# Kernel tuning notes

Hardware: AMD Instinct MI355X
Metric: run time of the kernel (lower is better)

Reference implementation:

```python
import jax, jax.numpy as jnp
import numpy as np

ATT, WEMB, VIEW, ADIM, EMB = 312, 512, 16, 2048, 2048
B = 2048
IN = ATT + WEMB + VIEW * WEMB  # 9016; output_dim defaults to input_dim
EPS = 1e-8  # torch cosine_similarity eps


def setup_inputs() -> dict:
    key = jax.random.key(0)
    ks = jax.random.split(key, 8)
    s = 0.02
    return {
        "x": jax.random.normal(ks[0], (B, IN), dtype=jnp.float32),
        "Wq": s * jax.random.normal(ks[1], (WEMB, ADIM), dtype=jnp.float32),
        "bq": jnp.zeros((ADIM,), jnp.float32),
        "Wk": s * jax.random.normal(ks[2], (WEMB, ADIM), dtype=jnp.float32),
        "bk": jnp.zeros((ADIM,), jnp.float32),
        "Wv": s * jax.random.normal(ks[3], (WEMB, ADIM), dtype=jnp.float32),
        "bv": jnp.zeros((ADIM,), jnp.float32),
        "Wm": s * jax.random.normal(ks[4], (ATT + ADIM, EMB), dtype=jnp.float32),
        "bm": jnp.zeros((EMB,), jnp.float32),
        "Wd1": s * jax.random.normal(ks[5], (EMB, 4096), dtype=jnp.float32),
        "bd1": jnp.zeros((4096,), jnp.float32),
        "Wd2": s * jax.random.normal(ks[6], (4096, IN), dtype=jnp.float32),
        "bd2": jnp.zeros((IN,), jnp.float32),
    }


def reference(x, Wq, bq, Wk, bk, Wv, bv, Wm, bm, Wd1, bd1, Wd2, bd2):
    att_emb = x[:, :ATT]                                   # [B, 312]
    desc_emb = x[:, ATT:ATT + WEMB]                        # [B, 512]
    gpt_emb = x[:, ATT + WEMB:].reshape(x.shape[0], -1, WEMB)  # [B, V, 512]

    # q is the same projected desc for every view (expand before linear)
    q = desc_emb @ Wq + bq                                 # [B, A]
    k = jnp.einsum("bvw,wa->bva", gpt_emb, Wk) + bk        # [B, V, A]
    v = jnp.einsum("bvw,wa->bva", gpt_emb, Wv) + bv        # [B, V, A]

    # cosed score: cosine similarity * L2 distance
    dot = jnp.einsum("bva,ba->bv", k, q)                   # [B, V]
    qn = jnp.maximum(jnp.linalg.norm(q, axis=-1), EPS)     # [B]
    kn = jnp.maximum(jnp.linalg.norm(k, axis=-1), EPS)     # [B, V]
    cs = dot / (qn[:, None] * kn)
    ed = jnp.linalg.norm(q[:, None, :] - k, axis=-1)       # [B, V]
    attn = jax.nn.softmax(cs * ed, axis=-1)                # [B, V]

    # torch.matmul([B,V], [B,V,A]) -> [B,B,A]; .mean(dim=1) averages over the
    # attn-batch axis, i.e. fused[j] = mean_b(attn[b]) @ v[j]. Compute the
    # mathematically identical form without the BxBxA intermediate.
    attn_mean = attn.mean(axis=0)                          # [V]
    fused = jnp.einsum("v,bva->ba", attn_mean, v)          # [B, A]

    z = jax.nn.relu(jnp.concatenate([att_emb, fused], axis=1) @ Wm + bm)  # [B, EMB]
    h = jax.nn.relu(z @ Wd1 + bd1)                          # [B, 4096]
    return h @ Wd2 + bd2                                    # [B, IN]
```

## Files before the change

kernel.cpp:

```cpp
#include <hip/hip_runtime.h>


typedef __bf16 bf16x8 __attribute__((ext_vector_type(8)));
typedef float  f32x4  __attribute__((ext_vector_type(4)));
typedef unsigned short u16;

#define ATT   312
#define WEMB  512
#define VIEW  16
#define ADIM  2048
#define EMB   2048
#define BATCH 2048
#define INDIM 9016
#define KCAT  2360
#define KCATP 2432
#define NOUT  9016
#define NOUTP 9216

__device__ __forceinline__ u16 f2bf(float f) {
  unsigned u = __builtin_bit_cast(unsigned, f);
  u += 0x7FFFu + ((u >> 16) & 1u);
  return (u16)(u >> 16);
}

__device__ __forceinline__ void gl_lds16(const u16* g, u16* l) {
  __builtin_amdgcn_global_load_lds((const __attribute__((address_space(1))) void*)g,
                                   (__attribute__((address_space(3))) void*)l, 16, 0, 0);
}

__global__ void castx_k(const float* __restrict__ x, u16* __restrict__ cc,
                        u16* __restrict__ desc, u16* __restrict__ gpt) {
  const int b = blockIdx.x, t = threadIdx.x;
  const float4* row = (const float4*)(x + (size_t)b * INDIM);
  for (int c = t; c < INDIM / 4; c += 256) {
    float4 v = row[c];
    ushort4 o = make_ushort4(f2bf(v.x), f2bf(v.y), f2bf(v.z), f2bf(v.w));
    if (c < ATT / 4)                 *(ushort4*)&cc[(size_t)b * KCATP + c * 4] = o;
    else if (c < (ATT + WEMB) / 4)   *(ushort4*)&desc[(size_t)b * WEMB + (c - ATT / 4) * 4] = o;
    else                             *(ushort4*)&gpt[(size_t)b * (VIEW * WEMB) + (c - (ATT + WEMB) / 4) * 4] = o;
  }
}

__global__ void transcast_k(const float* __restrict__ src, u16* __restrict__ dst,
                            int K, int N, int Kp, int Np) {
  __shared__ float tile[64][65];
  const int k0 = blockIdx.y * 64, n0 = blockIdx.x * 64;
  const int t = threadIdx.x;
  const int tr = t >> 4, tc4 = (t & 15) * 4;
#pragma unroll
  for (int i = 0; i < 4; ++i) {
    const int k = k0 + tr + i * 16;
    float v0 = 0.f, v1 = 0.f, v2 = 0.f, v3 = 0.f;
    if (k < K) {
      const int n = n0 + tc4;
      const float* p = src + (size_t)k * N + n;
      if (n + 3 < N) { float4 v = *(const float4*)p; v0 = v.x; v1 = v.y; v2 = v.z; v3 = v.w; }
      else {
        if (n + 0 < N) v0 = p[0];
        if (n + 1 < N) v1 = p[1];
        if (n + 2 < N) v2 = p[2];
        if (n + 3 < N) v3 = p[3];
      }
    }
    tile[tr + i * 16][tc4 + 0] = v0;
    tile[tr + i * 16][tc4 + 1] = v1;
    tile[tr + i * 16][tc4 + 2] = v2;
    tile[tr + i * 16][tc4 + 3] = v3;
  }
  __syncthreads();
#pragma unroll
  for (int i = 0; i < 4; ++i) {
    const int rn = tr + i * 16;
    const int n = n0 + rn;
    const int kk = k0 + tc4;
    if (n < Np) {
      const bool nv = (n < N);
      ushort4 o = make_ushort4(f2bf(nv ? tile[tc4 + 0][rn] : 0.f),
                               f2bf(nv ? tile[tc4 + 1][rn] : 0.f),
                               f2bf(nv ? tile[tc4 + 2][rn] : 0.f),
                               f2bf(nv ? tile[tc4 + 3][rn] : 0.f));
      *(ushort4*)&dst[(size_t)n * Kp + kk] = o;
    }
  }
}

__device__ __forceinline__ void stage_half(const u16* __restrict__ src, int ld,
                                           u16* dst, int wave, int lane) {
#pragma unroll
  for (int j = 0; j < 2; ++j) {
    const int s = wave * 2 + j;
    const int r = ((s >> 1) << 4) + (lane >> 2);
    const int c = ((s & 1) << 5) +
                  (((lane & 3) << 3) ^ (((lane >> 5) & 1) << 4));
    gl_lds16(src + (long)r * ld + c, dst + s * 512 + (lane << 3));
  }
}

#define BAR   __builtin_amdgcn_s_barrier()
#define LGKM0 asm volatile("s_waitcnt lgkmcnt(0)" ::: "memory")
#define VM6   asm volatile("s_waitcnt vmcnt(6)" ::: "memory")
#define VM0   asm volatile("s_waitcnt vmcnt(0)" ::: "memory")

#define RDA(bufo) do { _Pragma("unroll") for (int mf = 0; mf < 8; ++mf) \
  _Pragma("unroll") for (int kk = 0; kk < 2; ++kk) \
    a[mf][kk] = *(const bf16x8*)&lds[(bufo) + aoff0 + (mf * 2 + kk) * 512]; } while (0)
#define RDB(bufo, nfa, nfb) do { _Pragma("unroll") for (int nf = (nfa); nf <= (nfb); ++nf) \
  _Pragma("unroll") for (int kk = 0; kk < 2; ++kk) \
    b[nf][kk] = *(const bf16x8*)&lds[(bufo) + boff0 + nf * 1024 + kk * 512]; } while (0)
#define QUAD(qm, qn) do { __builtin_amdgcn_s_setprio(1); \
  _Pragma("unroll") for (int m4 = 0; m4 < 4; ++m4) \
  _Pragma("unroll") for (int n2 = 0; n2 < 2; ++n2) \
  _Pragma("unroll") for (int kk = 0; kk < 2; ++kk) \
    acc[(qm) * 4 + m4][(qn) * 2 + n2] = __builtin_amdgcn_mfma_f32_16x16x32_bf16( \
        a[(qm) * 4 + m4][kk], b[(qn) * 2 + n2][kk], acc[(qm) * 4 + m4][(qn) * 2 + n2], 0, 0, 0); \
  __builtin_amdgcn_s_setprio(0); } while (0)

template <int MODE, bool RELU>
__global__ __launch_bounds__(512, 2)
void gemm256(const u16* __restrict__ A, const u16* __restrict__ BT,
             const float* __restrict__ bias, int K, int Nreal,
             float* __restrict__ dstF, u16* __restrict__ dstH, int ldc,
             const float* __restrict__ qbuf, float* __restrict__ dotb,
             float* __restrict__ kn2b, int mt, int nt, int fastm) {
  __shared__ alignas(16) u16 lds[65536];
  const int nwg = mt * nt;
  const int xcd = blockIdx.x & 7, idx = blockIdx.x >> 3;
  const int qq = nwg >> 3, rr = nwg & 7;
  const int wg = (xcd < rr ? xcd * (qq + 1) : rr * (qq + 1) + (xcd - rr) * qq) + idx;
  int tm, tn;
  if (fastm) { tm = wg % mt; tn = wg / mt; } else { tn = wg % nt; tm = wg / nt; }

  const int tid = threadIdx.x;
  const int wave = tid >> 6, lane = tid & 63;
  const long m0 = (long)tm * 256, n0 = (long)tn * 256;
  const int wm = wave >> 2, wn = wave & 3;
  const u16* Ab = A + m0 * K;
  const u16* Bb = BT + n0 * K;

  f32x4 acc[8][4] = {};
  bf16x8 a[8][2], b[4][2];
  const int LP = (lane & 15) * 32 + ((((lane >> 4) << 3)) ^ (((lane >> 3) & 1) << 4));
  const int aoff0 = wm * 8192 + LP;
  const int boff0 = 16384 + (wn >> 1) * 8192 + (wn & 1) * 4096 + LP;
  const int NT = K >> 6;

  stage_half(Ab,               K, &lds[0],     wave, lane);
  stage_half(Ab + 128 * K,     K, &lds[8192],  wave, lane);
  stage_half(Bb,               K, &lds[16384], wave, lane);
  stage_half(Bb + 128 * K,     K, &lds[24576], wave, lane);
  stage_half(Ab + 64,          K, &lds[32768], wave, lane);
  stage_half(Ab + 128 * K + 64, K, &lds[40960], wave, lane);
  stage_half(Bb + 64,          K, &lds[49152], wave, lane);
  VM6; BAR;

  const int iters = NT >> 1;
  for (int i = 0; i < iters; ++i) {
    const int t0 = 2 * i;
    const bool nl = (i < iters - 1);
    RDA(0); RDB(0, 0, 1);
    stage_half(Bb + 128 * K + (t0 + 1) * 64, K, &lds[57344], wave, lane);
    BAR; LGKM0; QUAD(0, 0); BAR;
    RDB(0, 2, 3);
    if (nl) stage_half(Ab + (t0 + 2) * 64, K, &lds[0], wave, lane);
    BAR; LGKM0; QUAD(1, 0); BAR;
    if (nl) stage_half(Ab + 128 * K + (t0 + 2) * 64, K, &lds[8192], wave, lane);
    BAR; QUAD(0, 1); BAR;
    if (nl) stage_half(Bb + (t0 + 2) * 64, K, &lds[16384], wave, lane);
    BAR; QUAD(1, 1);
    if (nl) { VM6; } else { VM0; }
    BAR;
    RDA(32768); RDB(32768, 0, 1);
    if (nl) stage_half(Bb + 128 * K + (t0 + 2) * 64, K, &lds[24576], wave, lane);
    BAR; LGKM0; QUAD(0, 0); BAR;
    RDB(32768, 2, 3);
    if (nl) stage_half(Ab + (t0 + 3) * 64, K, &lds[32768], wave, lane);
    BAR; LGKM0; QUAD(1, 0); BAR;
    if (nl) stage_half(Ab + 128 * K + (t0 + 3) * 64, K, &lds[40960], wave, lane);
    BAR; QUAD(0, 1); BAR;
    if (nl) stage_half(Bb + (t0 + 3) * 64, K, &lds[49152], wave, lane);
    BAR; QUAD(1, 1);
    if (nl) VM6;
    BAR;
  }

  const int lr = lane >> 4, lc = lane & 15;
  if (MODE == 2) {
#pragma unroll
    for (int mf = 0; mf < 8; ++mf) {
#pragma unroll
      for (int r = 0; r < 4; ++r) {
        const long grow = m0 + wm * 128 + mf * 16 + lr * 4 + r;
        const long bb = grow >> 4;
        float ds = 0.f, ks = 0.f;
#pragma unroll
        for (int nf = 0; nf < 4; ++nf) {
          const long col = n0 + wn * 64 + nf * 16 + lc;
          float kv = acc[mf][nf][r] + bias[col];
          ds += kv * qbuf[bb * ADIM + col];
          ks += kv * kv;
        }
#pragma unroll
        for (int m = 1; m < 16; m <<= 1) {
          ds += __shfl_xor(ds, m, 64);
          ks += __shfl_xor(ks, m, 64);
        }
        if (lc == 0) {
          atomicAdd(&dotb[grow], ds);
          atomicAdd(&kn2b[grow], ks);
        }
      }
    }
  } else {
#pragma unroll
    for (int mf = 0; mf < 8; ++mf) {
#pragma unroll
      for (int nf = 0; nf < 4; ++nf) {
        const long col = n0 + wn * 64 + nf * 16 + lc;
        if (col < Nreal) {
          const float bv_ = bias[col];
#pragma unroll
          for (int r = 0; r < 4; ++r) {
            const long row = m0 + wm * 128 + mf * 16 + lr * 4 + r;
            float v = acc[mf][nf][r] + bv_;
            if (RELU) v = fmaxf(v, 0.f);
            if (MODE == 0) dstF[row * (long)ldc + col] = v;
            else           dstH[row * (long)ldc + col] = f2bf(v);
          }
        }
      }
    }
  }
}

template <int MODE, bool RELU>
__global__ __launch_bounds__(256, 2)
void gemm_bt(const u16* __restrict__ A, const u16* __restrict__ BT,
             const float* __restrict__ bias, int K, int Nreal,
             float* __restrict__ dstF, u16* __restrict__ dstH, int ldc,
             int mt, int nt, int fastm) {
  __shared__ alignas(16) u16 Ash[128 * 64];
  __shared__ alignas(16) u16 Bsh[128 * 64];
  const int nwg = mt * nt;
  const int xcd = blockIdx.x & 7, idx = blockIdx.x >> 3;
  const int qq = nwg >> 3, rr = nwg & 7;
  const int wg = (xcd < rr ? xcd * (qq + 1) : rr * (qq + 1) + (xcd - rr) * qq) + idx;
  int tm, tn;
  if (fastm) { tm = wg % mt; tn = wg / mt; } else { tn = wg % nt; tm = wg / nt; }

  const int tid = threadIdx.x;
  const int wave = tid >> 6, lane = tid & 63;
  const long m0 = (long)tm * 128;
  const long n0 = (long)tn * 128;
  const int wm = wave >> 1, wnn = wave & 1;
  f32x4 acc[4][4] = {};

  const int srow = (wave << 5) + (lane >> 3);
  const int scol = (lane & 7) << 3;

  for (int k0 = 0; k0 < K; k0 += 64) {
    __syncthreads();
#pragma unroll
    for (int i = 0; i < 4; ++i) {
      const int r = srow + i * 8;
      gl_lds16(A + (m0 + r) * (long)K + k0 + scol, &Ash[r * 64 + scol]);
      gl_lds16(BT + (n0 + r) * (long)K + k0 + scol, &Bsh[r * 64 + scol]);
    }
    __syncthreads();
#pragma unroll
    for (int kb = 0; kb < 2; ++kb) {
      bf16x8 af[4], bfv[4];
#pragma unroll
      for (int f = 0; f < 4; ++f) {
        af[f]  = *(const bf16x8*)&Ash[(wm * 64 + f * 16 + (lane & 15)) * 64 + kb * 32 + (lane >> 4) * 8];
        bfv[f] = *(const bf16x8*)&Bsh[(wnn * 64 + f * 16 + (lane & 15)) * 64 + kb * 32 + (lane >> 4) * 8];
      }
#pragma unroll
      for (int mf = 0; mf < 4; ++mf)
#pragma unroll
        for (int nf = 0; nf < 4; ++nf)
          acc[mf][nf] = __builtin_amdgcn_mfma_f32_16x16x32_bf16(af[mf], bfv[nf], acc[mf][nf], 0, 0, 0);
    }
  }

  const int lr = lane >> 4, lc = lane & 15;
#pragma unroll
  for (int mf = 0; mf < 4; ++mf) {
#pragma unroll
    for (int nf = 0; nf < 4; ++nf) {
      const long col = n0 + wnn * 64 + nf * 16 + lc;
      if (col < Nreal) {
        const float bv_ = bias[col];
#pragma unroll
        for (int r = 0; r < 4; ++r) {
          const long row = m0 + wm * 64 + mf * 16 + lr * 4 + r;
          float v = acc[mf][nf][r] + bv_;
          if (RELU) v = fmaxf(v, 0.f);
          if (MODE == 0) dstF[row * (long)ldc + col] = v;
          else           dstH[row * (long)ldc + col] = f2bf(v);
        }
      }
    }
  }
}

__global__ void qnorm_k(const float* __restrict__ q, float* __restrict__ qn2) {
  const int b = blockIdx.x, t = threadIdx.x;
  const float4* row = (const float4*)(q + (size_t)b * ADIM);
  float s = 0.f;
#pragma unroll
  for (int i = 0; i < 2; ++i) {
    float4 v = row[t + i * 256];
    s += v.x * v.x + v.y * v.y + v.z * v.z + v.w * v.w;
  }
#pragma unroll
  for (int m = 1; m < 64; m <<= 1) s += __shfl_xor(s, m, 64);
  __shared__ float wsum[4];
  if ((t & 63) == 0) wsum[t >> 6] = s;
  __syncthreads();
  if (t == 0) qn2[b] = wsum[0] + wsum[1] + wsum[2] + wsum[3];
}

__global__ void attn_k(const float* __restrict__ dotb, const float* __restrict__ kn2b,
                       const float* __restrict__ qn2, float* __restrict__ asum) {
  const int b = blockIdx.x * 256 + threadIdx.x;
  const int lane = threadIdx.x & 63;
  const float q2 = qn2[b];
  const float qn = fmaxf(sqrtf(q2), 1e-8f);
  float lg[VIEW];
  float mx = -1e30f;
#pragma unroll
  for (int v = 0; v < VIEW; ++v) {
    const float d = dotb[b * VIEW + v], k2 = kn2b[b * VIEW + v];
    const float kn = fmaxf(sqrtf(k2), 1e-8f);
    const float cs = d / (qn * kn);
    const float ed = sqrtf(fmaxf(q2 - 2.f * d + k2, 0.f));
    lg[v] = cs * ed;
    mx = fmaxf(mx, lg[v]);
  }
  float s = 0.f;
#pragma unroll
  for (int v = 0; v < VIEW; ++v) { lg[v] = expf(lg[v] - mx); s += lg[v]; }
  const float inv = 1.f / s;
#pragma unroll
  for (int v = 0; v < VIEW; ++v) {
    float aa = lg[v] * inv;
#pragma unroll
    for (int m = 1; m < 64; m <<= 1) aa += __shfl_xor(aa, m, 64);
    if (lane == 0) atomicAdd(&asum[v], aa);
  }
}

__global__ void gtilde_k(const u16* __restrict__ gpt, const float* __restrict__ asum,
                         u16* __restrict__ g) {
  const int b = blockIdx.x, t = threadIdx.x;
  float am[VIEW];
#pragma unroll
  for (int v = 0; v < VIEW; ++v) am[v] = asum[v] * (1.f / (float)BATCH);
  float s[8] = {};
  const u16* gx = gpt + (size_t)b * (VIEW * WEMB) + t * 8;
#pragma unroll
  for (int v = 0; v < VIEW; ++v) {
    bf16x8 gv = *(const bf16x8*)&gx[v * WEMB];
#pragma unroll
    for (int j = 0; j < 8; ++j) s[j] += am[v] * (float)gv[j];
  }
  ushort4 o0, o1;
  o0 = make_ushort4(f2bf(s[0]), f2bf(s[1]), f2bf(s[2]), f2bf(s[3]));
  o1 = make_ushort4(f2bf(s[4]), f2bf(s[5]), f2bf(s[6]), f2bf(s[7]));
  *(ushort4*)&g[(size_t)b * WEMB + t * 8] = o0;
  *(ushort4*)&g[(size_t)b * WEMB + t * 8 + 4] = o1;
}

extern "C" void kernel_launch(void* const* d_in, const int* in_sizes, int n_in,
                              void* d_out, int out_size, void* d_ws, size_t ws_size,
                              hipStream_t stream) {
  const float* x   = (const float*)d_in[0];
  const float* Wq  = (const float*)d_in[1];
  const float* bq  = (const float*)d_in[2];
  const float* Wk  = (const float*)d_in[3];
  const float* bk  = (const float*)d_in[4];
  const float* Wv  = (const float*)d_in[5];
  const float* bv  = (const float*)d_in[6];
  const float* Wm  = (const float*)d_in[7];
  const float* bm  = (const float*)d_in[8];
  const float* Wd1 = (const float*)d_in[9];
  const float* bd1 = (const float*)d_in[10];
  const float* Wd2 = (const float*)d_in[11];
  const float* bd2 = (const float*)d_in[12];
  float* out = (float*)d_out;

  char* ws = (char*)d_ws;
  size_t off = 0;
  auto alloc = [&](size_t bytes) -> void* {
    void* p = ws + off;
    off = (off + bytes + 255) & ~(size_t)255;
    return p;
  };
  u16* WqT  = (u16*)alloc((size_t)ADIM * WEMB * 2);
  u16* WkT  = (u16*)alloc((size_t)ADIM * WEMB * 2);
  u16* WvT  = (u16*)alloc((size_t)ADIM * WEMB * 2);
  u16* WmT  = (u16*)alloc((size_t)EMB * KCATP * 2);
  u16* Wd1T = (u16*)alloc((size_t)4096 * EMB * 2);
  u16* Wd2T = (u16*)alloc((size_t)NOUTP * 4096 * 2);
  u16* desc = (u16*)alloc((size_t)BATCH * WEMB * 2);
  u16* gpt  = (u16*)alloc((size_t)BATCH * VIEW * WEMB * 2);
  u16* cc   = (u16*)alloc((size_t)BATCH * KCATP * 2);
  float* q    = (float*)alloc((size_t)BATCH * ADIM * 4);
  float* qn2  = (float*)alloc((size_t)BATCH * 4);
  float* stats = (float*)alloc((size_t)(BATCH * VIEW * 2 + 64) * 4);
  float* dotb = stats;
  float* kn2b = stats + BATCH * VIEW;
  float* asum = stats + BATCH * VIEW * 2;
  u16* gt = (u16*)alloc((size_t)BATCH * WEMB * 2);
  u16* z  = (u16*)alloc((size_t)BATCH * EMB * 2);
  u16* h  = (u16*)alloc((size_t)BATCH * 4096 * 2);
  if (off > ws_size) return;

  hipMemsetAsync(stats, 0, (size_t)(BATCH * VIEW * 2 + 64) * 4, stream);
  hipMemsetAsync(cc, 0, (size_t)BATCH * KCATP * 2, stream);

  castx_k<<<BATCH, 256, 0, stream>>>(x, cc, desc, gpt);

  transcast_k<<<dim3(ADIM / 64, WEMB / 64), 256, 0, stream>>>(Wq, WqT, WEMB, ADIM, WEMB, ADIM);
  transcast_k<<<dim3(ADIM / 64, WEMB / 64), 256, 0, stream>>>(Wk, WkT, WEMB, ADIM, WEMB, ADIM);
  transcast_k<<<dim3(ADIM / 64, WEMB / 64), 256, 0, stream>>>(Wv, WvT, WEMB, ADIM, WEMB, ADIM);
  transcast_k<<<dim3(EMB / 64, KCATP / 64), 256, 0, stream>>>(Wm, WmT, KCAT, EMB, KCATP, EMB);
  transcast_k<<<dim3(4096 / 64, EMB / 64), 256, 0, stream>>>(Wd1, Wd1T, EMB, 4096, EMB, 4096);
  transcast_k<<<dim3(NOUTP / 64, 4096 / 64), 256, 0, stream>>>(Wd2, Wd2T, 4096, NOUT, 4096, NOUTP);

  gemm_bt<0, false><<<16 * 16, 256, 0, stream>>>(
      desc, WqT, bq, WEMB, ADIM, q, nullptr, ADIM, BATCH / 128, ADIM / 128, 0);
  qnorm_k<<<BATCH, 256, 0, stream>>>(q, qn2);
  gemm256<2, false><<<128 * 8, 512, 0, stream>>>(
      gpt, WkT, bk, WEMB, ADIM, nullptr, nullptr, 0, q, dotb, kn2b,
      BATCH * VIEW / 256, ADIM / 256, 0);
  attn_k<<<BATCH / 256, 256, 0, stream>>>(dotb, kn2b, qn2, asum);
  gtilde_k<<<BATCH, 64, 0, stream>>>(gpt, asum, gt);
  gemm_bt<1, false><<<16 * 16, 256, 0, stream>>>(
      gt, WvT, bv, WEMB, ADIM, nullptr, cc + ATT, KCATP, BATCH / 128, ADIM / 128, 0);
  gemm_bt<1, true><<<16 * 16, 256, 0, stream>>>(
      cc, WmT, bm, KCATP, EMB, nullptr, z, EMB, BATCH / 128, EMB / 128, 0);
  gemm256<1, true><<<8 * 16, 512, 0, stream>>>(
      z, Wd1T, bd1, EMB, 4096, nullptr, h, 4096, nullptr, nullptr, nullptr,
      BATCH / 256, 4096 / 256, 0);
  gemm256<0, false><<<8 * 36, 512, 0, stream>>>(
      h, Wd2T, bd2, 4096, NOUT, out, nullptr, NOUT, nullptr, nullptr, nullptr,
      BATCH / 256, NOUTP / 256, 1);
}
```

Measured before the change: 700.3 us.

## Split-K the two decoder GEMMs with fp32 atomic accumulation

Adds a K-split parameter to the 256x256 GEMM kernel so the Wd1 and Wd2 GEMMs launch 2x and 4x more workgroups. Each slice atomically adds its partial sums into a zeroed fp32 buffer, and only the first slice adds the bias. Because ReLU can no longer run in the epilogue, a separate kernel applies ReLU and casts the fp32 hidden activations to bf16. The aim is to fix poor CU occupancy and tail effects from the small tile counts, at the cost of extra memsets, atomic traffic, a larger fp32 intermediate that reuses the dead desc/gpt workspace, and nondeterministic summation order.

```diff
diff --git a/kernel.cpp b/kernel.cpp
--- a/kernel.cpp
+++ b/kernel.cpp
@@ -115,42 +115,45 @@
         a[(qm) * 4 + m4][kk], b[(qn) * 2 + n2][kk], acc[(qm) * 4 + m4][(qn) * 2 + n2], 0, 0, 0); \
   __builtin_amdgcn_s_setprio(0); } while (0)
 
-template <int MODE, bool RELU>
+template <int MODE>
 __global__ __launch_bounds__(512, 2)
 void gemm256(const u16* __restrict__ A, const u16* __restrict__ BT,
              const float* __restrict__ bias, int K, int Nreal,
-             float* __restrict__ dstF, u16* __restrict__ dstH, int ldc,
+             float* __restrict__ dstF, int ldc,
              const float* __restrict__ qbuf, float* __restrict__ dotb,
-             float* __restrict__ kn2b, int mt, int nt, int fastm) {
+             float* __restrict__ kn2b, int mt, int nt, int fastm,
+             int ks, int kl) {
   __shared__ alignas(16) u16 lds[65536];
-  const int nwg = mt * nt;
+  const int nwg = mt * nt * ks;
   const int xcd = blockIdx.x & 7, idx = blockIdx.x >> 3;
   const int qq = nwg >> 3, rr = nwg & 7;
   const int wg = (xcd < rr ? xcd * (qq + 1) : rr * (qq + 1) + (xcd - rr) * qq) + idx;
+  const int ksl = wg % ks;
+  const int rem = wg / ks;
   int tm, tn;
-  if (fastm) { tm = wg % mt; tn = wg / mt; } else { tn = wg % nt; tm = wg / nt; }
+  if (fastm) { tm = rem % mt; tn = rem / mt; } else { tn = rem % nt; tm = rem / nt; }
 
   const int tid = threadIdx.x;
   const int wave = tid >> 6, lane = tid & 63;
   const long m0 = (long)tm * 256, n0 = (long)tn * 256;
   const int wm = wave >> 2, wn = wave & 3;
-  const u16* Ab = A + m0 * K;
-  const u16* Bb = BT + n0 * K;
+  const u16* Ab = A + m0 * K + (long)ksl * kl;
+  const u16* Bb = BT + n0 * K + (long)ksl * kl;
 
   f32x4 acc[8][4] = {};
   bf16x8 a[8][2], b[4][2];
   const int LP = (lane & 15) * 32 + ((((lane >> 4) << 3)) ^ (((lane >> 3) & 1) << 4));
   const int aoff0 = wm * 8192 + LP;
   const int boff0 = 16384 + (wn >> 1) * 8192 + (wn & 1) * 4096 + LP;
-  const int NT = K >> 6;
-
-  stage_half(Ab,               K, &lds[0],     wave, lane);
-  stage_half(Ab + 128 * K,     K, &lds[8192],  wave, lane);
-  stage_half(Bb,               K, &lds[16384], wave, lane);
-  stage_half(Bb + 128 * K,     K, &lds[24576], wave, lane);
-  stage_half(Ab + 64,          K, &lds[32768], wave, lane);
+  const int NT = kl >> 6;
+
+  stage_half(Ab,                K, &lds[0],     wave, lane);
+  stage_half(Ab + 128 * K,      K, &lds[8192],  wave, lane);
+  stage_half(Bb,                K, &lds[16384], wave, lane);
+  stage_half(Bb + 128 * K,      K, &lds[24576], wave, lane);
+  stage_half(Ab + 64,           K, &lds[32768], wave, lane);
   stage_half(Ab + 128 * K + 64, K, &lds[40960], wave, lane);
-  stage_half(Bb + 64,          K, &lds[49152], wave, lane);
+  stage_half(Bb + 64,           K, &lds[49152], wave, lane);
   VM6; BAR;
 
   const int iters = NT >> 1;
@@ -191,22 +194,22 @@
       for (int r = 0; r < 4; ++r) {
         const long grow = m0 + wm * 128 + mf * 16 + lr * 4 + r;
         const long bb = grow >> 4;
-        float ds = 0.f, ks = 0.f;
+        float ds = 0.f, ks2 = 0.f;
 #pragma unroll
         for (int nf = 0; nf < 4; ++nf) {
           const long col = n0 + wn * 64 + nf * 16 + lc;
           float kv = acc[mf][nf][r] + bias[col];
           ds += kv * qbuf[bb * ADIM + col];
-          ks += kv * kv;
+          ks2 += kv * kv;
         }
 #pragma unroll
         for (int m = 1; m < 16; m <<= 1) {
           ds += __shfl_xor(ds, m, 64);
-          ks += __shfl_xor(ks, m, 64);
+          ks2 += __shfl_xor(ks2, m, 64);
         }
         if (lc == 0) {
           atomicAdd(&dotb[grow], ds);
-          atomicAdd(&kn2b[grow], ks);
+          atomicAdd(&kn2b[grow], ks2);
         }
       }
     }
@@ -217,19 +220,28 @@
       for (int nf = 0; nf < 4; ++nf) {
         const long col = n0 + wn * 64 + nf * 16 + lc;
         if (col < Nreal) {
-          const float bv_ = bias[col];
+          const float bv_ = (ksl == 0) ? bias[col] : 0.f;
 #pragma unroll
           for (int r = 0; r < 4; ++r) {
             const long row = m0 + wm * 128 + mf * 16 + lr * 4 + r;
-            float v = acc[mf][nf][r] + bv_;
-            if (RELU) v = fmaxf(v, 0.f);
-            if (MODE == 0) dstF[row * (long)ldc + col] = v;
-            else           dstH[row * (long)ldc + col] = f2bf(v);
+            atomicAdd(&dstF[row * (long)ldc + col], acc[mf][nf][r] + bv_);
           }
         }
       }
     }
   }
+}
+
+__global__ void relucast_k(const float* __restrict__ src, u16* __restrict__ dst) {
+  const int i = (blockIdx.x * 256 + threadIdx.x) * 8;
+  float4 va = *(const float4*)&src[i];
+  float4 vb = *(const float4*)&src[i + 4];
+  ushort4 o0 = make_ushort4(f2bf(fmaxf(va.x, 0.f)), f2bf(fmaxf(va.y, 0.f)),
+                            f2bf(fmaxf(va.z, 0.f)), f2bf(fmaxf(va.w, 0.f)));
+  ushort4 o1 = make_ushort4(f2bf(fmaxf(vb.x, 0.f)), f2bf(fmaxf(vb.y, 0.f)),
+                            f2bf(fmaxf(vb.z, 0.f)), f2bf(fmaxf(vb.w, 0.f)));
+  *(ushort4*)&dst[i] = o0;
+  *(ushort4*)&dst[i + 4] = o1;
 }
 
 template <int MODE, bool RELU>
@@ -415,7 +427,9 @@
   u16* z  = (u16*)alloc((size_t)BATCH * EMB * 2);
   u16* h  = (u16*)alloc((size_t)BATCH * 4096 * 2);
   if (off > ws_size) return;
-
+  float* h32 = (float*)desc;
+
+  hipMemsetAsync(out, 0, (size_t)out_size * 4, stream);
   hipMemsetAsync(stats, 0, (size_t)(BATCH * VIEW * 2 + 64) * 4, stream);
   hipMemsetAsync(cc, 0, (size_t)BATCH * KCATP * 2, stream);
 
@@ -431,19 +445,21 @@
   gemm_bt<0, false><<<16 * 16, 256, 0, stream>>>(
       desc, WqT, bq, WEMB, ADIM, q, nullptr, ADIM, BATCH / 128, ADIM / 128, 0);
   qnorm_k<<<BATCH, 256, 0, stream>>>(q, qn2);
-  gemm256<2, false><<<128 * 8, 512, 0, stream>>>(
-      gpt, WkT, bk, WEMB, ADIM, nullptr, nullptr, 0, q, dotb, kn2b,
-      BATCH * VIEW / 256, ADIM / 256, 0);
+  gemm256<2><<<128 * 8, 512, 0, stream>>>(
+      gpt, WkT, bk, WEMB, ADIM, nullptr, 0, q, dotb, kn2b,
+      BATCH * VIEW / 256, ADIM / 256, 0, 1, WEMB);
   attn_k<<<BATCH / 256, 256, 0, stream>>>(dotb, kn2b, qn2, asum);
   gtilde_k<<<BATCH, 64, 0, stream>>>(gpt, asum, gt);
   gemm_bt<1, false><<<16 * 16, 256, 0, stream>>>(
       gt, WvT, bv, WEMB, ADIM, nullptr, cc + ATT, KCATP, BATCH / 128, ADIM / 128, 0);
   gemm_bt<1, true><<<16 * 16, 256, 0, stream>>>(
       cc, WmT, bm, KCATP, EMB, nullptr, z, EMB, BATCH / 128, EMB / 128, 0);
-  gemm256<1, true><<<8 * 16, 512, 0, stream>>>(
-      z, Wd1T, bd1, EMB, 4096, nullptr, h, 4096, nullptr, nullptr, nullptr,
-      BATCH / 256, 4096 / 256, 0);
-  gemm256<0, false><<<8 * 36, 512, 0, stream>>>(
-      h, Wd2T, bd2, 4096, NOUT, out, nullptr, NOUT, nullptr, nullptr, nullptr,
-      BATCH / 256, NOUTP / 256, 1);
-}
+  hipMemsetAsync(h32, 0, (size_t)BATCH * 4096 * 4, stream);
+  gemm256<3><<<8 * 16 * 2, 512, 0, stream>>>(
+      z, Wd1T, bd1, EMB, 4096, h32, 4096, nullptr, nullptr, nullptr,
+      BATCH / 256, 4096 / 256, 1, 2, EMB / 2);
+  relucast_k<<<(BATCH * 4096) / 2048, 256, 0, stream>>>(h32, h);
+  gemm256<3><<<8 * 36 * 4, 512, 0, stream>>>(
+      h, Wd2T, bd2, 4096, NOUT, out, NOUT, nullptr, nullptr, nullptr,
+      BATCH / 256, NOUTP / 256, 1, 4, 1024);
+}
```

Measured after the change: 971.3 us. +38.7%, slower.
